# Kernel tuning notes

Hardware: AMD Instinct MI355X
Metric: run time of the kernel (lower is better)

## Reference

```python
import jax, jax.numpy as jnp
import numpy as np

B, H, W, C = 4, 64, 64, 32
M1 = M2 = 16
N = H * W          # 4096 grid nodes per sample
E = 131072         # edges (avg degree 32)
EDIM = 6           # edge feature dim
KMID = 64          # kernel MLP hidden width
EPS = 1e-5         # InstanceNorm eps


def _gelu(x):
    return jax.nn.gelu(x, approximate=False)  # torch nn.GELU default is exact erf


def _mlp(x, w1, b1, w2, b2):
    return _gelu(x @ w1 + b1) @ w2 + b2


def _inorm(x):
    # torch InstanceNorm2d(affine=False) applied to [B,H,W,C]: normalizes over last two dims
    m = x.mean(axis=(2, 3), keepdims=True)
    v = x.var(axis=(2, 3), keepdims=True)
    return (x - m) * jax.lax.rsqrt(v + EPS)


def _lin_init(k, fin, fout):
    lim = 1.0 / np.sqrt(fin)
    kw, kb = jax.random.split(k)
    w = jax.random.uniform(kw, (fin, fout), jnp.float32, -lim, lim)
    b = jax.random.uniform(kb, (fout,), jnp.float32, -lim, lim)
    return w, b


def setup_inputs() -> dict:
    key = jax.random.key(0)
    ks = jax.random.split(key, 14)
    s = 1.0 / (C * C)
    inp = {}
    inp['nodes'] = jax.random.normal(ks[0], (B, H, W, C), jnp.float32)
    inp['edge_index'] = jax.random.randint(ks[1], (2, E), 0, N, dtype=jnp.int64)
    inp['edge_attr'] = jax.random.uniform(ks[2], (E, EDIM), jnp.float32)
    # spectral conv complex weights, stored as real/imag float32 pairs
    inp['w1_re'] = s * jax.random.uniform(ks[3], (C, C, M1, M2), jnp.float32)
    inp['w1_im'] = s * jax.random.uniform(ks[4], (C, C, M1, M2), jnp.float32)
    inp['w2_re'] = s * jax.random.uniform(ks[5], (C, C, M1, M2), jnp.float32)
    inp['w2_im'] = s * jax.random.uniform(ks[6], (C, C, M1, M2), jnp.float32)
    # self.mlp : MLP(C, C, 2C)
    inp['mlp_w1'], inp['mlp_b1'] = _lin_init(ks[7], C, 2 * C)
    inp['mlp_w2'], inp['mlp_b2'] = _lin_init(ks[8], 2 * C, C)
    # self.w : MLP(C, C, 2C)
    inp['wm_w1'], inp['wm_b1'] = _lin_init(ks[9], C, 2 * C)
    inp['wm_w2'], inp['wm_b2'] = _lin_init(ks[10], 2 * C, C)
    # GNO kernel MLP : EDIM -> KMID -> C*C
    inp['ker_w1'], inp['ker_b1'] = _lin_init(ks[11], EDIM, KMID)
    inp['ker_w2'], inp['ker_b2'] = _lin_init(ks[12], KMID, C * C)
    # NNConv root weight and bias (PyG uniform(size) init with size=in_channels)
    lim = 1.0 / np.sqrt(C)
    kr, kb = jax.random.split(ks[13])
    inp['root'] = jax.random.uniform(kr, (C, C), jnp.float32, -lim, lim)
    inp['gbias'] = jax.random.uniform(kb, (C,), jnp.float32, -lim, lim)
    return inp


def reference(nodes, edge_index, edge_attr, w1_re, w1_im, w2_re, w2_im,
              mlp_w1, mlp_b1, mlp_w2, mlp_b2, wm_w1, wm_b1, wm_w2, wm_b2,
              ker_w1, ker_b1, ker_w2, ker_b2, root, gbias):
    x = _inorm(nodes)                                             # [B,H,W,C]

    # --- spectral conv branch ---
    x_ft = jnp.fft.rfftn(x, axes=(1, 2), norm='ortho')            # [B,H,W//2+1,C]
    w1 = (w1_re + 1j * w1_im).astype(jnp.complex64)
    w2 = (w2_re + 1j * w2_im).astype(jnp.complex64)
    top = jnp.einsum('bxyi,ioxy->bxyo', x_ft[:, :M1, :M2, :], w1)
    bot = jnp.einsum('bxyi,ioxy->bxyo', x_ft[:, -M1:, :M2, :], w2)
    out_ft = jnp.zeros((B, H, W // 2 + 1, C), jnp.complex64)
    out_ft = out_ft.at[:, :M1, :M2, :].set(top).at[:, -M1:, :M2, :].set(bot)
    x1 = jnp.fft.irfftn(out_ft, axes=(1, 2), s=(H, W), norm='ortho')
    x1 = _mlp(_inorm(x1), mlp_w1, mlp_b1, mlp_w2, mlp_b2)         # [B,H,W,C]

    # --- pointwise MLP branch ---
    x2 = _inorm(_mlp(x, wm_w1, wm_b1, wm_w2, wm_b2))              # [B,H,W,C]

    # --- edge-conditioned GNO branch ---
    x3 = x.reshape(B, N, C)
    wmat = _mlp(edge_attr, ker_w1, ker_b1, ker_w2, ker_b2).reshape(E, C, C)
    src, dst = edge_index[0], edge_index[1]
    msg = jnp.einsum('bec,eco->beo', x3[:, src, :], wmat)         # [B,E,C]
    agg = jnp.zeros((B, N, C), jnp.float32).at[:, dst, :].add(msg)
    x3 = agg + x3 @ root + gbias                                  # [B,N,C]

    return _gelu(x1 + x2 + x3.reshape(B, H, W, C))
```

## Files before the change

### kernel.cpp

```cpp
#include <hip/hip_runtime.h>

#define E_ 131072

typedef _Float16 half8 __attribute__((ext_vector_type(8)));
typedef float f32x4 __attribute__((ext_vector_type(4)));

__device__ __forceinline__ float gelu_f(float x) {
    return 0.5f * x * (1.0f + erff(x * 0.70710678118654752f));
}

#define TWOPI_64 (6.2831853071795864769f / 64.0f)

__device__ __forceinline__ void block_reduce2(float& s, float& s2, float* red) {
    #pragma unroll
    for (int off = 32; off > 0; off >>= 1) {
        s  += __shfl_down(s, off, 64);
        s2 += __shfl_down(s2, off, 64);
    }
    int lane = threadIdx.x & 63, wv = threadIdx.x >> 6;
    __syncthreads();
    if (lane == 0) { red[wv] = s; red[wv + 4] = s2; }
    __syncthreads();
    s  = red[0] + red[1] + red[2] + red[3];
    s2 = red[4] + red[5] + red[6] + red[7];
}

__device__ __forceinline__ void gno_body(int e0, float* sbufF, int* ssrc, int* sdst,
                                         const float* __restrict__ ea,
                                         const float* __restrict__ kw1, const float* __restrict__ kb1,
                                         const float* __restrict__ kb2,
                                         const _Float16* __restrict__ whi,
                                         const float* __restrict__ xn, const int* __restrict__ ei,
                                         float* __restrict__ agg) {
    _Float16* sxTh = (_Float16*)sbufF;
    int t = threadIdx.x;
    int lane = t & 63, wv = t >> 6, quad = lane >> 4, l15 = lane & 15;
    int eg = wv >> 1, t2 = wv & 1;

    if (t < 64) ssrc[t] = ei[e0 + t];
    else if (t < 128) sdst[t - 64] = ei[E_ + e0 + t - 64];
    {
        int r = t >> 2, k0 = (t & 3) * 16;
        const float* ep = ea + (e0 + r) * 6;
        float e6[6];
        #pragma unroll
        for (int d = 0; d < 6; ++d) e6[d] = ep[d];
        #pragma unroll
        for (int kk = 0; kk < 16; ++kk) {
            int k = k0 + kk;
            float acc = kb1[k];
            #pragma unroll
            for (int d = 0; d < 6; ++d) acc += e6[d] * kw1[d * 64 + k];
            sbufF[r * 68 + k] = gelu_f(acc);
        }
    }
    __syncthreads();
    half8 ahi[2][2], alo[2][2];
    #pragma unroll
    for (int et = 0; et < 2; ++et) {
        #pragma unroll
        for (int kh = 0; kh < 2; ++kh) {
            const float* hp = sbufF + (eg * 32 + et * 16 + l15) * 68 + kh * 32 + quad * 8;
            float4 h0 = *(const float4*)hp;
            float4 h1 = *(const float4*)(hp + 4);
            float hv[8] = {h0.x, h0.y, h0.z, h0.w, h1.x, h1.y, h1.z, h1.w};
            half8 hh, hl;
            #pragma unroll
            for (int j = 0; j < 8; ++j) {
                _Float16 hi = (_Float16)hv[j];
                hh[j] = hi;
                hl[j] = (_Float16)(hv[j] - (float)hi);
            }
            ahi[et][kh] = hh;
            alo[et][kh] = hl;
        }
    }
    __syncthreads();
    {
        int b = t & 3, r = t >> 2;
        int s = ssrc[r];
        int pe = (r >> 5) * 32 + ((r >> 2) & 3) * 8 + ((r >> 4) & 1) * 4 + (r & 3);
        const float4* xp = (const float4*)(xn + (b * 4096 + s) * 32);
        _Float16* dp = sxTh + b * 2312 + pe;
        #pragma unroll
        for (int q = 0; q < 8; ++q) {
            float4 v = xp[q];
            dp[(q * 4 + 0) * 72] = (_Float16)v.x;
            dp[(q * 4 + 1) * 72] = (_Float16)v.y;
            dp[(q * 4 + 2) * 72] = (_Float16)v.z;
            dp[(q * 4 + 3) * 72] = (_Float16)v.w;
        }
    }
    __syncthreads();
    float msg[4][2][4];
    #pragma unroll
    for (int b = 0; b < 4; ++b)
        #pragma unroll
        for (int et = 0; et < 2; ++et)
            #pragma unroll
            for (int r = 0; r < 4; ++r) msg[b][et][r] = 0.f;

    for (int i = 0; i < 32; ++i) {
        float b2v = kb2[i * 32 + t2 * 16 + l15];
        int f0 = (i * 4 + t2 * 2) * 512 + lane * 8;
        half8 bhi0 = *(const half8*)(whi + f0);
        half8 bhi1 = *(const half8*)(whi + f0 + 512);
        f32x4 acc[2];
        #pragma unroll
        for (int et = 0; et < 2; ++et) {
            f32x4 ac = {b2v, b2v, b2v, b2v};
            ac = __builtin_amdgcn_mfma_f32_16x16x32_f16(ahi[et][0], bhi0, ac, 0, 0, 0);
            ac = __builtin_amdgcn_mfma_f32_16x16x32_f16(ahi[et][1], bhi1, ac, 0, 0, 0);
            ac = __builtin_amdgcn_mfma_f32_16x16x32_f16(alo[et][0], bhi0, ac, 0, 0, 0);
            ac = __builtin_amdgcn_mfma_f32_16x16x32_f16(alo[et][1], bhi1, ac, 0, 0, 0);
            acc[et] = ac;
        }
        #pragma unroll
        for (int b = 0; b < 4; ++b) {
            const half8 xv = *(const half8*)(sxTh + b * 2312 + i * 72 + eg * 32 + quad * 8);
            #pragma unroll
            for (int et = 0; et < 2; ++et) {
                msg[b][et][0] += (float)xv[et * 4 + 0] * acc[et][0];
                msg[b][et][1] += (float)xv[et * 4 + 1] * acc[et][1];
                msg[b][et][2] += (float)xv[et * 4 + 2] * acc[et][2];
                msg[b][et][3] += (float)xv[et * 4 + 3] * acc[et][3];
            }
        }
    }
    int o = t2 * 16 + l15;
    #pragma unroll
    for (int et = 0; et < 2; ++et) {
        #pragma unroll
        for (int r = 0; r < 4; ++r) {
            int row = eg * 32 + et * 16 + quad * 4 + r;
            int d = sdst[row];
            #pragma unroll
            for (int b = 0; b < 4; ++b) {
                atomicAdd(&agg[(b * 4096 + d) * 32 + o], msg[b][et][r]);
            }
        }
    }
}

__global__ __launch_bounds__(256, 4) void k_pre(const float* __restrict__ nodes,
                                                const float* __restrict__ w2,
                                                float* __restrict__ xn,
                                                float* __restrict__ agg,
                                                float* __restrict__ Gre, float* __restrict__ Gim,
                                                _Float16* __restrict__ whi) {
    int t = threadIdx.x;
    if (blockIdx.x >= 256) {
        int g0 = (blockIdx.x - 256) * 512 + t;
        #pragma unroll 1
        for (int rep = 0; rep < 2; ++rep) {
            int g = g0 + rep * 256;
            int j = g & 7, l = (g >> 3) & 63, fid = g >> 9;
            int i = fid >> 2, t2 = (fid >> 1) & 1, kh = fid & 1;
            int quad = l >> 4, l15 = l & 15;
            int k = kh * 32 + quad * 8 + j;
            int n = i * 32 + t2 * 16 + l15;
            whi[g] = (_Float16)w2[k * 1024 + n];
        }
        return;
    }
    int bh = blockIdx.x;
    __shared__ float sx[2048];
    __shared__ float tc[64], ts[64];
    __shared__ float red[8];
    const float4* src = (const float4*)(nodes + bh * 2048);
    float4* dst = (float4*)(xn + bh * 2048);
    float4* az = (float4*)(agg + bh * 2048);
    if (t < 64) { float a = TWOPI_64 * t; tc[t] = cosf(a); ts[t] = sinf(a); }
    float4 v0 = src[t * 2], v1 = src[t * 2 + 1];
    float s  = v0.x + v0.y + v0.z + v0.w + v1.x + v1.y + v1.z + v1.w;
    float s2 = v0.x*v0.x + v0.y*v0.y + v0.z*v0.z + v0.w*v0.w
             + v1.x*v1.x + v1.y*v1.y + v1.z*v1.z + v1.w*v1.w;
    block_reduce2(s, s2, red);
    float mean = s * (1.0f / 2048.0f);
    float var  = s2 * (1.0f / 2048.0f) - mean * mean;
    float sc = rsqrtf(var + 1e-5f);
    v0.x = (v0.x - mean) * sc; v0.y = (v0.y - mean) * sc;
    v0.z = (v0.z - mean) * sc; v0.w = (v0.w - mean) * sc;
    v1.x = (v1.x - mean) * sc; v1.y = (v1.y - mean) * sc;
    v1.z = (v1.z - mean) * sc; v1.w = (v1.w - mean) * sc;
    dst[t * 2] = v0; dst[t * 2 + 1] = v1;
    float4 z = {0.f, 0.f, 0.f, 0.f};
    az[t * 2] = z; az[t * 2 + 1] = z;
    ((float4*)sx)[t * 2] = v0;
    ((float4*)sx)[t * 2 + 1] = v1;
    __syncthreads();
    #pragma unroll 1
    for (int rep = 0; rep < 2; ++rep) {
        int oi = rep * 256 + t;
        int ky = oi >> 5, i = oi & 31;
        float re = 0.f, im = 0.f;
        #pragma unroll 8
        for (int w = 0; w < 64; ++w) {
            float v = sx[w * 32 + i];
            int m = (ky * w) & 63;
            re += v * tc[m];
            im -= v * ts[m];
        }
        Gre[bh * 512 + oi] = re;
        Gim[bh * 512 + oi] = im;
    }
}

__global__ __launch_bounds__(256, 4) void k_g1(
        const float* __restrict__ Gre, const float* __restrict__ Gim,
        const float* __restrict__ w1re, const float* __restrict__ w1im,
        const float* __restrict__ w2re, const float* __restrict__ w2im,
        float* __restrict__ Yr, float* __restrict__ Yi,
        const float* __restrict__ ww1, const float* __restrict__ wb1,
        const float* __restrict__ ww2, const float* __restrict__ wb2,
        float* __restrict__ osum,
        const float* __restrict__ ea,
        const float* __restrict__ kw1, const float* __restrict__ kb1,
        const float* __restrict__ kb2,
        const _Float16* __restrict__ whi,
        const float* __restrict__ xn,
        const int* __restrict__ ei,
        float* __restrict__ agg) {
    __shared__ __align__(16) float U[4624];
    __shared__ int ssrc[64], sdst[64];
    int t = threadIdx.x;

    if (blockIdx.x < 128) {
        float* tc  = U;
        float* ts  = U + 64;
        float* sXr = U + 128;
        float* sXi = U + 656;
        int bid = blockIdx.x;
        int b = bid >> 5, kxi = bid & 31;
        int kx = kxi + (kxi < 16 ? 0 : 32);
        int x = kxi & 15;
        const float* wre = (kxi < 16) ? w1re : w2re;
        const float* wim = (kxi < 16) ? w1im : w2im;
        if (t < 64) { float a = TWOPI_64 * t; tc[t] = cosf(a); ts[t] = sinf(a); }
        __syncthreads();
        #pragma unroll 1
        for (int rep = 0; rep < 2; ++rep) {
            int oi = rep * 256 + t;
            int ky = oi >> 5, i = oi & 31;
            float re = 0.f, im = 0.f;
            #pragma unroll 8
            for (int h = 0; h < 64; ++h) {
                int gidx = (b * 64 + h) * 512 + ky * 32 + i;
                float gr = Gre[gidx], gi = Gim[gidx];
                int m = (kx * h) & 63;
                float c = tc[m], sv = ts[m];
                re += gr * c + gi * sv;
                im += gi * c - gr * sv;
            }
            sXr[ky * 33 + i] = re;
            sXi[ky * 33 + i] = im;
        }
        __syncthreads();
        #pragma unroll 1
        for (int rep = 0; rep < 2; ++rep) {
            int oi = rep * 256 + t;
            int ky = oi & 15, o = oi >> 4;
            float re = 0.f, im = 0.f;
            #pragma unroll 4
            for (int i = 0; i < 32; ++i) {
                float xr = sXr[ky * 33 + i], xi = sXi[ky * 33 + i];
                int widx = (i * 32 + o) * 256 + x * 16 + ky;
                float wr = wre[widx], wi = wim[widx];
                re += xr * wr - xi * wi;
                im += xr * wi + xi * wr;
            }
            Yr[bid * 512 + ky * 32 + o] = re;
            Yi[bid * 512 + ky * 32 + o] = im;
        }
        return;
    }
    if (blockIdx.x < 384) {
        int bh = blockIdx.x - 128;
        float* red = U;
        float* sX = U + 8;
        _Float16* sHh = (_Float16*)(U + 2120);
        for (int f = t; f < 2048; f += 256) sX[(f >> 5) * 33 + (f & 31)] = xn[bh * 2048 + f];
        __syncthreads();
        #pragma unroll 1
        for (int rep = 0; rep < 16; ++rep) {
            int idx = rep * 256 + t;
            int w = idx >> 6, k = idx & 63;
            float acc = wb1[k];
            #pragma unroll 4
            for (int c = 0; c < 32; ++c) acc += sX[w * 33 + c] * ww1[c * 64 + k];
            sHh[w * 72 + k] = (_Float16)gelu_f(acc);
        }
        __syncthreads();
        float s = 0.f, s2 = 0.f;
        #pragma unroll 1
        for (int rep = 0; rep < 8; ++rep) {
            int idx = rep * 256 + t;
            int w = idx >> 5, o = idx & 31;
            float acc = wb2[o];
            #pragma unroll 4
            for (int k = 0; k < 64; ++k) acc += (float)sHh[w * 72 + k] * ww2[k * 32 + o];
            sX[w * 33 + o] = acc;
            s += acc; s2 += acc * acc;
        }
        block_reduce2(s, s2, red);
        float mean = s * (1.0f / 2048.0f);
        float sc = rsqrtf(s2 * (1.0f / 2048.0f) - mean * mean + 1e-5f);
        #pragma unroll 1
        for (int rep = 0; rep < 8; ++rep) {
            int idx = rep * 256 + t;
            int w = idx >> 5, o = idx & 31;
            osum[bh * 2048 + idx] = (sX[w * 33 + o] - mean) * sc;
        }
        return;
    }
    gno_body((blockIdx.x - 384) * 64, U, ssrc, sdst,
             ea, kw1, kb1, kb2, whi, xn, ei, agg);
}

__global__ __launch_bounds__(256, 4) void k_g2(
        const float* __restrict__ Yr, const float* __restrict__ Yi,
        const float* __restrict__ mw1, const float* __restrict__ mb1,
        const float* __restrict__ mw2, const float* __restrict__ mb2,
        float* __restrict__ osum) {
    __shared__ __align__(16) float U[4624];
    int t = threadIdx.x;

    int bh = blockIdx.x;
    int b = bh >> 6, h = bh & 63;
    float* red = U;
    float* sP  = U + 8;
    float* sZr = U + 2120;
    float* sZi = U + 2648;
    float* tc  = U + 3176;
    float* ts  = U + 3240;
    _Float16* sHh = (_Float16*)(U + 2120);
    if (t < 64) { float a = TWOPI_64 * t; tc[t] = cosf(a); ts[t] = sinf(a); }
    __syncthreads();
    #pragma unroll 1
    for (int rep = 0; rep < 2; ++rep) {
        int oi = rep * 256 + t;
        int ky = oi >> 5, o = oi & 31;
        float re = 0.f, im = 0.f;
        #pragma unroll 4
        for (int kxi = 0; kxi < 32; ++kxi) {
            int kx = kxi + (kxi < 16 ? 0 : 32);
            int m = (kx * h) & 63;
            float c = tc[m], sv = ts[m];
            int yidx = (b * 32 + kxi) * 512 + ky * 32 + o;
            float yr = Yr[yidx], yi = Yi[yidx];
            re += yr * c - yi * sv;
            im += yr * sv + yi * c;
        }
        sZr[ky * 33 + o] = re;
        sZi[ky * 33 + o] = im;
    }
    __syncthreads();
    float s = 0.f, s2 = 0.f;
    #pragma unroll 1
    for (int rep = 0; rep < 8; ++rep) {
        int idx = rep * 256 + t;
        int w = idx >> 5, o = idx & 31;
        float acc = sZr[o];
        #pragma unroll
        for (int ky = 1; ky < 16; ++ky) {
            int m = (ky * w) & 63;
            acc += 2.0f * (sZr[ky * 33 + o] * tc[m] - sZi[ky * 33 + o] * ts[m]);
        }
        acc *= (1.0f / 4096.0f);
        sP[w * 33 + o] = acc;
        s += acc; s2 += acc * acc;
    }
    block_reduce2(s, s2, red);
    float mean = s * (1.0f / 2048.0f);
    float sc = rsqrtf(s2 * (1.0f / 2048.0f) - mean * mean + 1e-5f);
    #pragma unroll 1
    for (int rep = 0; rep < 8; ++rep) {
        int idx = rep * 256 + t;
        int w = idx >> 5, o = idx & 31;
        sP[w * 33 + o] = (sP[w * 33 + o] - mean) * sc;
    }
    __syncthreads();
    #pragma unroll 1
    for (int rep = 0; rep < 16; ++rep) {
        int idx = rep * 256 + t;
        int w = idx >> 6, k = idx & 63;
        float acc = mb1[k];
        #pragma unroll 4
        for (int c = 0; c < 32; ++c) acc += sP[w * 33 + c] * mw1[c * 64 + k];
        sHh[w * 72 + k] = (_Float16)gelu_f(acc);
    }
    __syncthreads();
    #pragma unroll 1
    for (int rep = 0; rep < 8; ++rep) {
        int idx = rep * 256 + t;
        int w = idx >> 5, o = idx & 31;
        float acc = mb2[o];
        #pragma unroll 4
        for (int k = 0; k < 64; ++k) acc += (float)sHh[w * 72 + k] * mw2[k * 32 + o];
        osum[bh * 2048 + idx] += acc;
    }
}

__global__ __launch_bounds__(256, 4) void k_final(const float* __restrict__ osum, const float* __restrict__ agg,
                                                  const float* __restrict__ xn, const float* __restrict__ root,
                                                  const float* __restrict__ gbias, float* __restrict__ out) {
    int bh = blockIdx.x >> 2, q = blockIdx.x & 3;
    int base = bh * 2048 + q * 512;
    int t = threadIdx.x;
    __shared__ float sX[16 * 33];
    __shared__ float sR[1024];
    for (int f = t; f < 512; f += 256) sX[(f >> 5) * 33 + (f & 31)] = xn[base + f];
    for (int f = t; f < 1024; f += 256) sR[f] = root[f];
    __syncthreads();
    #pragma unroll 1
    for (int rep = 0; rep < 2; ++rep) {
        int idx = rep * 256 + t;
        int w = idx >> 5, o = idx & 31;
        float acc = gbias[o] + osum[base + idx] + agg[base + idx];
        #pragma unroll 4
        for (int c = 0; c < 32; ++c) acc += sX[w * 33 + c] * sR[c * 32 + o];
        out[base + idx] = gelu_f(acc);
    }
}

extern "C" void kernel_launch(void* const* d_in, const int* in_sizes, int n_in,
                              void* d_out, int out_size, void* d_ws, size_t ws_size,
                              hipStream_t stream) {
    (void)in_sizes; (void)n_in; (void)out_size; (void)ws_size;
    const float* nodes  = (const float*)d_in[0];
    const int*   eidx   = (const int*)d_in[1];
    const float* eattr  = (const float*)d_in[2];
    const float* w1re   = (const float*)d_in[3];
    const float* w1im   = (const float*)d_in[4];
    const float* w2re   = (const float*)d_in[5];
    const float* w2im   = (const float*)d_in[6];
    const float* mlp_w1 = (const float*)d_in[7];
    const float* mlp_b1 = (const float*)d_in[8];
    const float* mlp_w2 = (const float*)d_in[9];
    const float* mlp_b2 = (const float*)d_in[10];
    const float* wm_w1  = (const float*)d_in[11];
    const float* wm_b1  = (const float*)d_in[12];
    const float* wm_w2  = (const float*)d_in[13];
    const float* wm_b2  = (const float*)d_in[14];
    const float* ker_w1 = (const float*)d_in[15];
    const float* ker_b1 = (const float*)d_in[16];
    const float* ker_w2 = (const float*)d_in[17];
    const float* ker_b2 = (const float*)d_in[18];
    const float* root   = (const float*)d_in[19];
    const float* gbias  = (const float*)d_in[20];
    float* out = (float*)d_out;

    char* ws = (char*)d_ws;
    size_t off = 0;
    auto alloc = [&](size_t bytes) {
        void* p = ws + off;
        off += (bytes + 255) & ~(size_t)255;
        return p;
    };
    float* xn   = (float*)alloc(524288 * 4);
    float* agg  = (float*)alloc(524288 * 4);
    float* osum = (float*)alloc(524288 * 4);
    float* Gre  = (float*)alloc(131072 * 4);
    float* Gim  = (float*)alloc(131072 * 4);
    float* Yr   = (float*)alloc(65536 * 4);
    float* Yi   = (float*)alloc(65536 * 4);
    _Float16* whi = (_Float16*)alloc(65536 * 2);

    k_pre<<<384, 256, 0, stream>>>(nodes, ker_w2, xn, agg, Gre, Gim, whi);
    k_g1<<<2432, 256, 0, stream>>>(Gre, Gim, w1re, w1im, w2re, w2im, Yr, Yi,
                                   wm_w1, wm_b1, wm_w2, wm_b2, osum,
                                   eattr, ker_w1, ker_b1, ker_b2, whi, xn, eidx, agg);
    k_g2<<<256, 256, 0, stream>>>(Yr, Yi, mlp_w1, mlp_b1, mlp_w2, mlp_b2, osum);
    k_final<<<1024, 256, 0, stream>>>(osum, agg, xn, root, gbias, out);
}
```

Before: 242.7 us.

## Fuse final epilogue into k_g2 and split k_pre DFT rows across two blocks

```diff
diff --git a/kernel.cpp b/kernel.cpp
--- a/kernel.cpp
+++ b/kernel.cpp
@@ -149,8 +149,8 @@
                                                 float* __restrict__ Gre, float* __restrict__ Gim,
                                                 _Float16* __restrict__ whi) {
     int t = threadIdx.x;
-    if (blockIdx.x >= 256) {
-        int g0 = (blockIdx.x - 256) * 512 + t;
+    if (blockIdx.x >= 512) {
+        int g0 = (blockIdx.x - 512) * 512 + t;
         #pragma unroll 1
         for (int rep = 0; rep < 2; ++rep) {
             int g = g0 + rep * 256;
@@ -163,13 +163,12 @@
         }
         return;
     }
-    int bh = blockIdx.x;
+    int bh = blockIdx.x & 255;
+    int drep = blockIdx.x >> 8;
     __shared__ float sx[2048];
     __shared__ float tc[64], ts[64];
     __shared__ float red[8];
     const float4* src = (const float4*)(nodes + bh * 2048);
-    float4* dst = (float4*)(xn + bh * 2048);
-    float4* az = (float4*)(agg + bh * 2048);
     if (t < 64) { float a = TWOPI_64 * t; tc[t] = cosf(a); ts[t] = sinf(a); }
     float4 v0 = src[t * 2], v1 = src[t * 2 + 1];
     float s  = v0.x + v0.y + v0.z + v0.w + v1.x + v1.y + v1.z + v1.w;
@@ -183,15 +182,18 @@
     v0.z = (v0.z - mean) * sc; v0.w = (v0.w - mean) * sc;
     v1.x = (v1.x - mean) * sc; v1.y = (v1.y - mean) * sc;
     v1.z = (v1.z - mean) * sc; v1.w = (v1.w - mean) * sc;
-    dst[t * 2] = v0; dst[t * 2 + 1] = v1;
-    float4 z = {0.f, 0.f, 0.f, 0.f};
-    az[t * 2] = z; az[t * 2 + 1] = z;
+    if (drep == 0) {
+        float4* dst = (float4*)(xn + bh * 2048);
+        float4* az = (float4*)(agg + bh * 2048);
+        dst[t * 2] = v0; dst[t * 2 + 1] = v1;
+        float4 z = {0.f, 0.f, 0.f, 0.f};
+        az[t * 2] = z; az[t * 2 + 1] = z;
+    }
     ((float4*)sx)[t * 2] = v0;
     ((float4*)sx)[t * 2 + 1] = v1;
     __syncthreads();
-    #pragma unroll 1
-    for (int rep = 0; rep < 2; ++rep) {
-        int oi = rep * 256 + t;
+    {
+        int oi = drep * 256 + t;
         int ky = oi >> 5, i = oi & 31;
         float re = 0.f, im = 0.f;
         #pragma unroll 8
@@ -317,23 +319,36 @@
              ea, kw1, kb1, kb2, whi, xn, ei, agg);
 }
 
-__global__ __launch_bounds__(256, 4) void k_g2(
+__global__ __launch_bounds__(256, 4) void k_g2f(
         const float* __restrict__ Yr, const float* __restrict__ Yi,
         const float* __restrict__ mw1, const float* __restrict__ mb1,
         const float* __restrict__ mw2, const float* __restrict__ mb2,
-        float* __restrict__ osum) {
-    __shared__ __align__(16) float U[4624];
+        const float* __restrict__ osum, const float* __restrict__ agg,
+        const float* __restrict__ xn, const float* __restrict__ root,
+        const float* __restrict__ gbias, float* __restrict__ out) {
+    __shared__ __align__(16) float U[8744];
     int t = threadIdx.x;
-
     int bh = blockIdx.x;
     int b = bh >> 6, h = bh & 63;
-    float* red = U;
-    float* sP  = U + 8;
-    float* sZr = U + 2120;
-    float* sZi = U + 2648;
-    float* tc  = U + 3176;
-    float* ts  = U + 3240;
-    _Float16* sHh = (_Float16*)(U + 2120);
+    float* tc  = U;
+    float* ts  = U + 64;
+    float* red = U + 128;
+    float* sZr = U + 136;
+    float* sZi = U + 664;
+    float* sP  = U + 1192;
+    _Float16* sHh = (_Float16*)(U + 3304);
+    float* sX  = U + 5608;
+    float* sR  = U + 7720;
+
+    for (int f = t; f < 2048; f += 256) sX[(f >> 5) * 33 + (f & 31)] = xn[bh * 2048 + f];
+    for (int f = t; f < 1024; f += 256) sR[f] = root[f];
+    float osv[8], agv[8];
+    #pragma unroll
+    for (int rep = 0; rep < 8; ++rep) {
+        int idx = rep * 256 + t;
+        osv[rep] = osum[bh * 2048 + idx];
+        agv[rep] = agg[bh * 2048 + idx];
+    }
     if (t < 64) { float a = TWOPI_64 * t; tc[t] = cosf(a); ts[t] = sinf(a); }
     __syncthreads();
     #pragma unroll 1
@@ -394,32 +409,13 @@
     for (int rep = 0; rep < 8; ++rep) {
         int idx = rep * 256 + t;
         int w = idx >> 5, o = idx & 31;
-        float acc = mb2[o];
+        float x1v = mb2[o];
         #pragma unroll 4
-        for (int k = 0; k < 64; ++k) acc += (float)sHh[w * 72 + k] * mw2[k * 32 + o];
-        osum[bh * 2048 + idx] += acc;
-    }
-}
-
-__global__ __launch_bounds__(256, 4) void k_final(const float* __restrict__ osum, const float* __restrict__ agg,
-                                                  const float* __restrict__ xn, const float* __restrict__ root,
-                                                  const float* __restrict__ gbias, float* __restrict__ out) {
-    int bh = blockIdx.x >> 2, q = blockIdx.x & 3;
-    int base = bh * 2048 + q * 512;
-    int t = threadIdx.x;
-    __shared__ float sX[16 * 33];
-    __shared__ float sR[1024];
-    for (int f = t; f < 512; f += 256) sX[(f >> 5) * 33 + (f & 31)] = xn[base + f];
-    for (int f = t; f < 1024; f += 256) sR[f] = root[f];
-    __syncthreads();
-    #pragma unroll 1
-    for (int rep = 0; rep < 2; ++rep) {
-        int idx = rep * 256 + t;
-        int w = idx >> 5, o = idx & 31;
-        float acc = gbias[o] + osum[base + idx] + agg[base + idx];
+        for (int k = 0; k < 64; ++k) x1v += (float)sHh[w * 72 + k] * mw2[k * 32 + o];
+        float val = gbias[o] + osv[rep] + agv[rep] + x1v;
         #pragma unroll 4
-        for (int c = 0; c < 32; ++c) acc += sX[w * 33 + c] * sR[c * 32 + o];
-        out[base + idx] = gelu_f(acc);
+        for (int c = 0; c < 32; ++c) val += sX[w * 33 + c] * sR[c * 32 + o];
+        out[bh * 2048 + idx] = gelu_f(val);
     }
 }
 
@@ -466,10 +462,10 @@
     float* Yi   = (float*)alloc(65536 * 4);
     _Float16* whi = (_Float16*)alloc(65536 * 2);
 
-    k_pre<<<384, 256, 0, stream>>>(nodes, ker_w2, xn, agg, Gre, Gim, whi);
+    k_pre<<<640, 256, 0, stream>>>(nodes, ker_w2, xn, agg, Gre, Gim, whi);
     k_g1<<<2432, 256, 0, stream>>>(Gre, Gim, w1re, w1im, w2re, w2im, Yr, Yi,
                                    wm_w1, wm_b1, wm_w2, wm_b2, osum,
                                    eattr, ker_w1, ker_b1, ker_b2, whi, xn, eidx, agg);
-    k_g2<<<256, 256, 0, stream>>>(Yr, Yi, mlp_w1, mlp_b1, mlp_w2, mlp_b2, osum);
-    k_final<<<1024, 256, 0, stream>>>(osum, agg, xn, root, gbias, out);
-}
+    k_g2f<<<256, 256, 0, stream>>>(Yr, Yi, mlp_w1, mlp_b1, mlp_w2, mlp_b2,
+                                   osum, agg, xn, root, gbias, out);
+}
```

Measured after the change: 238.4 us. Within noise of the previous version (-1.8%).
